# Kernel optimization log

Hardware: AMD Instinct MI355X
Metric: run time of the kernel (lower is better)

## Reference

```python
import jax, jax.numpy as jnp
import numpy as np

H = 1024      # hidden_size
NH = 16       # num heads
HD = H // NH  # head dim


def setup_inputs() -> dict:
    key = jax.random.key(0)
    ks = jax.random.split(key, 10)
    B, S = 2, 2048
    bound = 1.0 / np.sqrt(H)
    def w(k):
        return jax.random.uniform(k, (H, H), jnp.float32, -bound, bound)
    def b(k):
        return jax.random.uniform(k, (H,), jnp.float32, -bound, bound)
    return {
        "hidden_states": jax.random.normal(ks[0], (B, S, H), jnp.float32),
        "attention_mask": jnp.zeros((B, 1, 1, S), jnp.float32),
        "wq": w(ks[1]), "bq": b(ks[2]),
        "wk": w(ks[3]), "bk": b(ks[4]),
        "wv": w(ks[5]), "bv": b(ks[6]),
        "wo": w(ks[7]), "bo": b(ks[8]),
    }


def reference(hidden_states, attention_mask, wq, bq, wk, bk, wv, bv, wo, bo):
    B, S, _ = hidden_states.shape
    # linear layers: y = x @ W^T + b (torch F.linear convention)
    q = hidden_states @ wq.T + bq
    k = hidden_states @ wk.T + bk
    v = hidden_states @ wv.T + bv
    # [B, NH, S, HD]
    q = q.reshape(B, S, NH, HD).transpose(0, 2, 1, 3)
    k = k.reshape(B, S, NH, HD).transpose(0, 2, 1, 3)
    v = v.reshape(B, S, NH, HD).transpose(0, 2, 1, 3)
    scores = jnp.einsum("bhqd,bhkd->bhqk", q, k) / jnp.sqrt(jnp.float32(HD))
    scores = scores + attention_mask
    probs = jax.nn.softmax(scores, axis=-1)  # dropout_p=0 -> no dropout
    ctx = jnp.einsum("bhqk,bhkd->bhqd", probs, v)
    ctx = ctx.transpose(0, 2, 1, 3).reshape(B, S, H)
    return ctx @ wo.T + bo
```

## Files before the change

### kernel.cpp

```cpp
#include <hip/hip_runtime.h>
#include <hip/hip_bf16.h>

typedef unsigned short u16;
typedef __attribute__((ext_vector_type(4))) float f32x4;
typedef __attribute__((ext_vector_type(8))) __bf16 bf16x8;

#define NH 16
#define HD 64
#define HID 1024
#define SS 2048
#define MM 4096

__device__ __forceinline__ u16 f2b(float f) {
  unsigned u = __builtin_bit_cast(unsigned, f);
  u += 0x7fff + ((u >> 16) & 1);
  return (u16)(u >> 16);
}

__device__ __forceinline__ float fexp2(float x) {
#if __has_builtin(__builtin_amdgcn_exp2f)
  return __builtin_amdgcn_exp2f(x);
#else
  return exp2f(x);
#endif
}

template <int CTRL>
__device__ __forceinline__ float dpp_mv(float x) {
  int xi = __builtin_bit_cast(int, x);
  int yi = __builtin_amdgcn_update_dpp(xi, xi, CTRL, 0xF, 0xF, true);
  return __builtin_bit_cast(float, yi);
}
__device__ __forceinline__ float dppmax16(float v) {
  v = fmaxf(v, dpp_mv<0xB1>(v));
  v = fmaxf(v, dpp_mv<0x4E>(v));
  v = fmaxf(v, dpp_mv<0x141>(v));
  v = fmaxf(v, dpp_mv<0x140>(v));
  return v;
}
__device__ __forceinline__ float dppsum16(float v) {
  v += dpp_mv<0xB1>(v);
  v += dpp_mv<0x4E>(v);
  v += dpp_mv<0x141>(v);
  v += dpp_mv<0x140>(v);
  return v;
}

__device__ __forceinline__ void gl_lds16(const u16* g, u16* l) {
  __builtin_amdgcn_global_load_lds(
      (const __attribute__((address_space(1))) void*)g,
      (__attribute__((address_space(3))) void*)l, 16, 0, 0);
}

__global__ void cvt4(const float* __restrict__ src, u16* __restrict__ dst, int n4) {
  int i = blockIdx.x * 256 + threadIdx.x;
  if (i >= n4) return;
  float4 v = reinterpret_cast<const float4*>(src)[i];
  ushort4 o;
  o.x = f2b(v.x); o.y = f2b(v.y); o.z = f2b(v.z); o.w = f2b(v.w);
  reinterpret_cast<ushort4*>(dst)[i] = o;
}

__global__ void cvt4w(const float* __restrict__ s0, const float* __restrict__ s1,
                      const float* __restrict__ s2, const float* __restrict__ s3,
                      u16* __restrict__ d0, u16* __restrict__ d1,
                      u16* __restrict__ d2, u16* __restrict__ d3) {
  const int w = blockIdx.y;
  const float* src = (w == 0) ? s0 : (w == 1) ? s1 : (w == 2) ? s2 : s3;
  u16* dst = (w == 0) ? d0 : (w == 1) ? d1 : (w == 2) ? d2 : d3;
  int i = blockIdx.x * 256 + threadIdx.x;
  float4 v = reinterpret_cast<const float4*>(src)[i];
  ushort4 o;
  o.x = f2b(v.x); o.y = f2b(v.y); o.z = f2b(v.z); o.w = f2b(v.w);
  reinterpret_cast<ushort4*>(dst)[i] = o;
}

__global__ __launch_bounds__(256)
void gemm_qkv(const u16* __restrict__ xb,
              const u16* __restrict__ wqb, const u16* __restrict__ wkb, const u16* __restrict__ wvb,
              const float* __restrict__ bq, const float* __restrict__ bk, const float* __restrict__ bv,
              u16* __restrict__ qh, u16* __restrict__ kh, u16* __restrict__ vt) {
  const int mt = blockIdx.x;
  const int nt = blockIdx.y;
  const int wi = nt >> 3;
  const int n0 = (nt & 7) << 7;
  const int m0 = mt << 7;
  const u16* wb = (wi == 0) ? wqb : (wi == 1) ? wkb : wvb;
  const float* bias = (wi == 0) ? bq : (wi == 1) ? bk : bv;

  __shared__ u16 at[128 * 64];
  __shared__ u16 bt[128 * 64];

  const int tid = threadIdx.x;
  const int wave = tid >> 6;
  const int lane = tid & 63;
  const int g = lane >> 4;
  const int wm = (wave >> 1) << 6;
  const int wn = (wave & 1) << 6;
  const int lr = lane & 15;
  const int rb = g << 2;
  const int lrow = lane >> 3;
  const int dslot = lane & 7;

  f32x4 acc[4][4] = {};

  for (int k0 = 0; k0 < HID; k0 += 64) {
    __syncthreads();
    #pragma unroll
    for (int i = 0; i < 4; i++) {
      const int row = wave * 32 + i * 8 + lrow;
      const int scol = (dslot ^ (row & 7)) << 3;
      gl_lds16(&xb[(size_t)(m0 + row) * HID + k0 + scol], at + wave * 2048 + i * 512);
      gl_lds16(&wb[(size_t)(n0 + row) * HID + k0 + scol], bt + wave * 2048 + i * 512);
    }
    __syncthreads();
    #pragma unroll
    for (int kk = 0; kk < 2; kk++) {
      bf16x8 af[4], bfr[4];
      #pragma unroll
      for (int i = 0; i < 4; i++) {
        const int ra = wm + i * 16 + lr;
        const int rbw = wn + i * 16 + lr;
        const int sa_ = ((kk << 2) + g) ^ (ra & 7);
        const int sb_ = ((kk << 2) + g) ^ (rbw & 7);
        af[i]  = *reinterpret_cast<const bf16x8*>(&at[ra * 64 + (sa_ << 3)]);
        bfr[i] = *reinterpret_cast<const bf16x8*>(&bt[rbw * 64 + (sb_ << 3)]);
      }
      #pragma unroll
      for (int i = 0; i < 4; i++)
        #pragma unroll
        for (int j = 0; j < 4; j++)
          acc[i][j] = __builtin_amdgcn_mfma_f32_16x16x32_bf16(af[i], bfr[j], acc[i][j], 0, 0, 0);
    }
  }

  #pragma unroll
  for (int i = 0; i < 4; i++) {
    #pragma unroll
    for (int j = 0; j < 4; j++) {
      #pragma unroll
      for (int r = 0; r < 4; r++) {
        const int m = m0 + wm + i * 16 + rb + r;
        const int n = n0 + wn + j * 16 + lr;
        const float val = acc[i][j][r] + bias[n];
        const u16 bv16 = f2b(val);
        const int b = m >> 11, s = m & 2047;
        const int h = n >> 6, d = n & 63;
        if (wi == 0)      qh[((size_t)(b * NH + h) * SS + s) * HD + d] = bv16;
        else if (wi == 1) kh[((size_t)(b * NH + h) * SS + s) * HD + d] = bv16;
        else              vt[((size_t)(b * NH + h) * HD + d) * SS + s] = bv16;
      }
    }
  }
}

__global__ __launch_bounds__(256, 2)
void attn(const u16* __restrict__ qh, const u16* __restrict__ kh, const u16* __restrict__ vt,
          const float* __restrict__ mask, u16* __restrict__ ctxb) {
  const int id = blockIdx.x;
  const int bh = (id & 7) + 8 * ((id >> 3) & 3);
  const int qt = id >> 5;
  const int b = bh >> 4;
  const int h = bh & 15;
  const int q0 = qt << 7;

  const int tid = threadIdx.x;
  const int wave = tid >> 6;
  const int lane = tid & 63;
  const int g = lane >> 4;
  const int lr = lane & 15;
  const int lk = g << 3;
  const int rb = g << 2;
  const int lrow = lane >> 3;
  const int dslot = lane & 7;

  const u16* qb = qh + (size_t)bh * SS * HD;
  const u16* kb = kh + (size_t)bh * SS * HD;
  const u16* vb = vt + (size_t)bh * HD * SS;
  const float* mrow = mask + (size_t)b * SS;

  __shared__ u16 kt[2][64 * 64];
  __shared__ u16 vtile[2][64 * 64];
  __shared__ u16 pt[4][32][72];

  const int qrow0 = q0 + wave * 32;

  bf16x8 qf[2][2];
  #pragma unroll
  for (int c = 0; c < 2; c++)
    #pragma unroll
    for (int dk = 0; dk < 2; dk++)
      qf[c][dk] = *reinterpret_cast<const bf16x8*>(
          &qb[(size_t)(qrow0 + c * 16 + lr) * HD + dk * 32 + lk]);

  f32x4 o[2][4] = {};
  float mrun[2][4], lrun[2][4];
  #pragma unroll
  for (int c = 0; c < 2; c++)
    #pragma unroll
    for (int r = 0; r < 4; r++) { mrun[c][r] = -1e30f; lrun[c][r] = 0.f; }

  const float LOG2E = 1.4426950408889634f;
  const float SCL = 0.125f * LOG2E;

  auto stage = [&](u16* kdst, u16* vdst, int kv0) {
    #pragma unroll
    for (int i = 0; i < 2; i++) {
      const int row = wave * 16 + i * 8 + lrow;
      const int scol = (dslot ^ (row & 7)) << 3;
      gl_lds16(&kb[(size_t)(kv0 + row) * HD + scol], kdst + wave * 1024 + i * 512);
      gl_lds16(&vb[(size_t)row * SS + kv0 + scol], vdst + wave * 1024 + i * 512);
    }
  };

  stage(kt[0], vtile[0], 0);
  __syncthreads();

  for (int it = 0; it < SS / 64; ++it) {
    const int cur = it & 1;
    if (it + 1 < SS / 64)
      stage(kt[cur ^ 1], vtile[cur ^ 1], (it + 1) * 64);

    const int kv0 = it * 64;
    const u16* kc = kt[cur];
    const u16* vc = vtile[cur];

    f32x4 sa[2][4] = {};
    #pragma unroll
    for (int ks = 0; ks < 4; ks++) {
      const int row = ks * 16 + lr;
      const int s0 = g ^ (row & 7);
      const int s1 = (g + 4) ^ (row & 7);
      const bf16x8 kf0 = *reinterpret_cast<const bf16x8*>(&kc[row * 64 + (s0 << 3)]);
      const bf16x8 kf1 = *reinterpret_cast<const bf16x8*>(&kc[row * 64 + (s1 << 3)]);
      #pragma unroll
      for (int c = 0; c < 2; c++) {
        sa[c][ks] = __builtin_amdgcn_mfma_f32_16x16x32_bf16(qf[c][0], kf0, sa[c][ks], 0, 0, 0);
        sa[c][ks] = __builtin_amdgcn_mfma_f32_16x16x32_bf16(qf[c][1], kf1, sa[c][ks], 0, 0, 0);
      }
    }

    float mk2[4];
    #pragma unroll
    for (int ks = 0; ks < 4; ks++) mk2[ks] = mrow[kv0 + ks * 16 + lr] * LOG2E;

    float tmax[2][4];
    #pragma unroll
    for (int c = 0; c < 2; c++) {
      #pragma unroll
      for (int r = 0; r < 4; r++) tmax[c][r] = -1e30f;
      #pragma unroll
      for (int ks = 0; ks < 4; ks++)
        #pragma unroll
        for (int r = 0; r < 4; r++) {
          const float v = fmaf(sa[c][ks][r], SCL, mk2[ks]);
          sa[c][ks][r] = v;
          tmax[c][r] = fmaxf(tmax[c][r], v);
        }
      #pragma unroll
      for (int r = 0; r < 4; r++) tmax[c][r] = dppmax16(tmax[c][r]);
    }

    float need = -1e30f;
    #pragma unroll
    for (int c = 0; c < 2; c++)
      #pragma unroll
      for (int r = 0; r < 4; r++) need = fmaxf(need, tmax[c][r] - mrun[c][r]);
    if (!__all(need <= 4.0f)) {
      #pragma unroll
      for (int c = 0; c < 2; c++)
        #pragma unroll
        for (int r = 0; r < 4; r++) {
          const float mnew = fmaxf(mrun[c][r], tmax[c][r]);
          const float alpha = fexp2(mrun[c][r] - mnew);
          mrun[c][r] = mnew;
          lrun[c][r] *= alpha;
          #pragma unroll
          for (int ds = 0; ds < 4; ds++) o[c][ds][r] *= alpha;
        }
    }

    #pragma unroll
    for (int c = 0; c < 2; c++) {
      float ts[4] = {0.f, 0.f, 0.f, 0.f};
      #pragma unroll
      for (int ks = 0; ks < 4; ks++)
        #pragma unroll
        for (int r = 0; r < 4; r++) {
          const float p = fexp2(sa[c][ks][r] - mrun[c][r]);
          sa[c][ks][r] = p;
          ts[r] += p;
        }
      #pragma unroll
      for (int r = 0; r < 4; r++)
        lrun[c][r] += dppsum16(ts[r]);
      #pragma unroll
      for (int ks = 0; ks < 4; ks++)
        #pragma unroll
        for (int r = 0; r < 4; r++)
          pt[wave][c * 16 + rb + r][ks * 16 + lr] = f2b(sa[c][ks][r]);
    }

    bf16x8 pa[2][2];
    #pragma unroll
    for (int c = 0; c < 2; c++)
      #pragma unroll
      for (int ko = 0; ko < 2; ko++)
        pa[c][ko] = *reinterpret_cast<const bf16x8*>(&pt[wave][c * 16 + lr][ko * 32 + lk]);

    #pragma unroll
    for (int ds = 0; ds < 4; ds++) {
      #pragma unroll
      for (int ko = 0; ko < 2; ko++) {
        const int vrow = ds * 16 + lr;
        const int vs = ((ko << 2) + g) ^ (vrow & 7);
        const bf16x8 vf = *reinterpret_cast<const bf16x8*>(&vc[vrow * 64 + (vs << 3)]);
        #pragma unroll
        for (int c = 0; c < 2; c++)
          o[c][ds] = __builtin_amdgcn_mfma_f32_16x16x32_bf16(pa[c][ko], vf, o[c][ds], 0, 0, 0);
      }
    }
    __syncthreads();
  }

  #pragma unroll
  for (int c = 0; c < 2; c++) {
    float inv[4];
    #pragma unroll
    for (int r = 0; r < 4; r++) inv[r] = 1.0f / lrun[c][r];
    #pragma unroll
    for (int ds = 0; ds < 4; ds++)
      #pragma unroll
      for (int r = 0; r < 4; r++) {
        const int srow = qrow0 + c * 16 + rb + r;
        ctxb[(size_t)(b * SS + srow) * HID + h * HD + ds * 16 + lr] = f2b(o[c][ds][r] * inv[r]);
      }
  }
}

__global__ __launch_bounds__(256)
void gemm_out(const u16* __restrict__ ab, const u16* __restrict__ wb,
              const float* __restrict__ bias, float* __restrict__ out) {
  const int m0 = blockIdx.x << 7;
  const int n0 = blockIdx.y << 6;

  __shared__ u16 at[128 * 32];
  __shared__ u16 bt[64 * 32];

  const int tid = threadIdx.x;
  const int wave = tid >> 6;
  const int lane = tid & 63;
  const int wm = wave << 5;
  const int lr = lane & 15;
  const int lk = (lane >> 4) << 3;
  const int rb = (lane >> 4) << 2;

  const int srow = wave * 32 + (lane >> 2);
  const int brow = wave * 16 + (lane >> 2);
  const int scol = (lane & 3) << 3;
  const size_t ga0 = (size_t)(m0 + srow) * HID + scol;
  const size_t gb0 = (size_t)(n0 + brow) * HID + scol;
  u16* la0 = at + wave * 1024;
  u16* lb0 = bt + wave * 512;

  f32x4 acc[2][4] = {};

  for (int k0 = 0; k0 < HID; k0 += 32) {
    __syncthreads();
    gl_lds16(&ab[ga0 + k0], la0);
    gl_lds16(&ab[ga0 + 16 * HID + k0], la0 + 512);
    gl_lds16(&wb[gb0 + k0], lb0);
    __syncthreads();
    bf16x8 af[2], bfr[4];
    #pragma unroll
    for (int i = 0; i < 2; i++)
      af[i] = *reinterpret_cast<const bf16x8*>(&at[(wm + i * 16 + lr) * 32 + lk]);
    #pragma unroll
    for (int j = 0; j < 4; j++)
      bfr[j] = *reinterpret_cast<const bf16x8*>(&bt[(j * 16 + lr) * 32 + lk]);
    #pragma unroll
    for (int i = 0; i < 2; i++)
      #pragma unroll
      for (int j = 0; j < 4; j++)
        acc[i][j] = __builtin_amdgcn_mfma_f32_16x16x32_bf16(af[i], bfr[j], acc[i][j], 0, 0, 0);
  }

  #pragma unroll
  for (int i = 0; i < 2; i++)
    #pragma unroll
    for (int j = 0; j < 4; j++)
      #pragma unroll
      for (int r = 0; r < 4; r++) {
        const int m = m0 + wm + i * 16 + rb + r;
        const int n = n0 + j * 16 + lr;
        out[(size_t)m * HID + n] = acc[i][j][r] + bias[n];
      }
}

extern "C" void kernel_launch(void* const* d_in, const int* in_sizes, int n_in,
                              void* d_out, int out_size, void* d_ws, size_t ws_size,
                              hipStream_t stream) {
  const float* hs   = (const float*)d_in[0];
  const float* mask = (const float*)d_in[1];
  const float* wq   = (const float*)d_in[2];
  const float* bq   = (const float*)d_in[3];
  const float* wk   = (const float*)d_in[4];
  const float* bk   = (const float*)d_in[5];
  const float* wv   = (const float*)d_in[6];
  const float* bv   = (const float*)d_in[7];
  const float* wo   = (const float*)d_in[8];
  const float* bo   = (const float*)d_in[9];
  float* out = (float*)d_out;

  char* ws = (char*)d_ws;
  u16* xb   = (u16*)(ws);
  u16* ctxb = (u16*)(ws + ((size_t)8  << 20));
  u16* qhb  = (u16*)(ws + ((size_t)16 << 20));
  u16* khb  = (u16*)(ws + ((size_t)24 << 20));
  u16* vtb  = (u16*)(ws + ((size_t)32 << 20));
  u16* wqb  = (u16*)(ws + ((size_t)40 << 20));
  u16* wkb  = (u16*)(ws + ((size_t)42 << 20));
  u16* wvb  = (u16*)(ws + ((size_t)44 << 20));
  u16* wob  = (u16*)(ws + ((size_t)46 << 20));

  cvt4<<<4096, 256, 0, stream>>>(hs, xb, MM * HID / 4);
  cvt4w<<<dim3(1024, 4), 256, 0, stream>>>(wq, wk, wv, wo, wqb, wkb, wvb, wob);

  gemm_qkv<<<dim3(32, 24), 256, 0, stream>>>(xb, wqb, wkb, wvb, bq, bk, bv, qhb, khb, vtb);
  attn<<<512, 256, 0, stream>>>(qhb, khb, vtb, mask, ctxb);
  gemm_out<<<dim3(32, 16), 256, 0, stream>>>(ctxb, wob, bo, out);
}
```

Baseline: 162.3 us.

## Defer softmax row reductions and widen output GEMM K-tile with swizzled LDS

In the attention kernel, the cross-lane row max is computed only when the rescale branch fires. The row sum is kept per lane and reduced once at the end, and P is written to shared memory directly without the temporary. The output projection GEMM now loads 64-wide K tiles into XOR-swizzled LDS, halving loop iterations and barriers and avoiding bank conflicts. The intent is to cut DPP reduction work and synchronization overhead, at the price of more LDS use. The rescale check now runs on lane-local maxima, which looks safe because the full row max is recomputed when the branch is taken.

```diff
diff --git a/kernel.cpp b/kernel.cpp
--- a/kernel.cpp
+++ b/kernel.cpp
@@ -257,8 +257,6 @@
           sa[c][ks][r] = v;
           tmax[c][r] = fmaxf(tmax[c][r], v);
         }
-      #pragma unroll
-      for (int r = 0; r < 4; r++) tmax[c][r] = dppmax16(tmax[c][r]);
     }
 
     float need = -1e30f;
@@ -271,7 +269,8 @@
       for (int c = 0; c < 2; c++)
         #pragma unroll
         for (int r = 0; r < 4; r++) {
-          const float mnew = fmaxf(mrun[c][r], tmax[c][r]);
+          const float rowmax = dppmax16(tmax[c][r]);
+          const float mnew = fmaxf(mrun[c][r], rowmax);
           const float alpha = fexp2(mrun[c][r] - mnew);
           mrun[c][r] = mnew;
           lrun[c][r] *= alpha;
@@ -281,25 +280,15 @@
     }
 
     #pragma unroll
-    for (int c = 0; c < 2; c++) {
-      float ts[4] = {0.f, 0.f, 0.f, 0.f};
+    for (int c = 0; c < 2; c++)
       #pragma unroll
       for (int ks = 0; ks < 4; ks++)
         #pragma unroll
         for (int r = 0; r < 4; r++) {
           const float p = fexp2(sa[c][ks][r] - mrun[c][r]);
-          sa[c][ks][r] = p;
-          ts[r] += p;
+          lrun[c][r] += p;
+          pt[wave][c * 16 + rb + r][ks * 16 + lr] = f2b(p);
         }
-      #pragma unroll
-      for (int r = 0; r < 4; r++)
-        lrun[c][r] += dppsum16(ts[r]);
-      #pragma unroll
-      for (int ks = 0; ks < 4; ks++)
-        #pragma unroll
-        for (int r = 0; r < 4; r++)
-          pt[wave][c * 16 + rb + r][ks * 16 + lr] = f2b(sa[c][ks][r]);
-    }
 
     bf16x8 pa[2][2];
     #pragma unroll
@@ -327,7 +316,7 @@
   for (int c = 0; c < 2; c++) {
     float inv[4];
     #pragma unroll
-    for (int r = 0; r < 4; r++) inv[r] = 1.0f / lrun[c][r];
+    for (int r = 0; r < 4; r++) inv[r] = 1.0f / dppsum16(lrun[c][r]);
     #pragma unroll
     for (int ds = 0; ds < 4; ds++)
       #pragma unroll
@@ -344,45 +333,57 @@
   const int m0 = blockIdx.x << 7;
   const int n0 = blockIdx.y << 6;
 
-  __shared__ u16 at[128 * 32];
-  __shared__ u16 bt[64 * 32];
+  __shared__ u16 at[128 * 64];
+  __shared__ u16 bt[64 * 64];
 
   const int tid = threadIdx.x;
   const int wave = tid >> 6;
   const int lane = tid & 63;
+  const int g = lane >> 4;
   const int wm = wave << 5;
   const int lr = lane & 15;
-  const int lk = (lane >> 4) << 3;
-  const int rb = (lane >> 4) << 2;
-
-  const int srow = wave * 32 + (lane >> 2);
-  const int brow = wave * 16 + (lane >> 2);
-  const int scol = (lane & 3) << 3;
-  const size_t ga0 = (size_t)(m0 + srow) * HID + scol;
-  const size_t gb0 = (size_t)(n0 + brow) * HID + scol;
-  u16* la0 = at + wave * 1024;
-  u16* lb0 = bt + wave * 512;
+  const int rb = g << 2;
+  const int lrow = lane >> 3;
+  const int dslot = lane & 7;
 
   f32x4 acc[2][4] = {};
 
-  for (int k0 = 0; k0 < HID; k0 += 32) {
+  for (int k0 = 0; k0 < HID; k0 += 64) {
     __syncthreads();
-    gl_lds16(&ab[ga0 + k0], la0);
-    gl_lds16(&ab[ga0 + 16 * HID + k0], la0 + 512);
-    gl_lds16(&wb[gb0 + k0], lb0);
+    #pragma unroll
+    for (int i = 0; i < 4; i++) {
+      const int row = wave * 32 + i * 8 + lrow;
+      const int scol = (dslot ^ (row & 7)) << 3;
+      gl_lds16(&ab[(size_t)(m0 + row) * HID + k0 + scol], at + wave * 2048 + i * 512);
+    }
+    #pragma unroll
+    for (int i = 0; i < 2; i++) {
+      const int row = wave * 16 + i * 8 + lrow;
+      const int scol = (dslot ^ (row & 7)) << 3;
+      gl_lds16(&wb[(size_t)(n0 + row) * HID + k0 + scol], bt + wave * 1024 + i * 512);
+    }
     __syncthreads();
-    bf16x8 af[2], bfr[4];
-    #pragma unroll
-    for (int i = 0; i < 2; i++)
-      af[i] = *reinterpret_cast<const bf16x8*>(&at[(wm + i * 16 + lr) * 32 + lk]);
-    #pragma unroll
-    for (int j = 0; j < 4; j++)
-      bfr[j] = *reinterpret_cast<const bf16x8*>(&bt[(j * 16 + lr) * 32 + lk]);
-    #pragma unroll
-    for (int i = 0; i < 2; i++)
-      #pragma unroll
-      for (int j = 0; j < 4; j++)
-        acc[i][j] = __builtin_amdgcn_mfma_f32_16x16x32_bf16(af[i], bfr[j], acc[i][j], 0, 0, 0);
+    #pragma unroll
+    for (int kk = 0; kk < 2; kk++) {
+      bf16x8 af[2], bfr[4];
+      #pragma unroll
+      for (int i = 0; i < 2; i++) {
+        const int ra = wm + i * 16 + lr;
+        const int sa_ = ((kk << 2) + g) ^ (ra & 7);
+        af[i] = *reinterpret_cast<const bf16x8*>(&at[ra * 64 + (sa_ << 3)]);
+      }
+      #pragma unroll
+      for (int j = 0; j < 4; j++) {
+        const int rbw = j * 16 + lr;
+        const int sb_ = ((kk << 2) + g) ^ (rbw & 7);
+        bfr[j] = *reinterpret_cast<const bf16x8*>(&bt[rbw * 64 + (sb_ << 3)]);
+      }
+      #pragma unroll
+      for (int i = 0; i < 2; i++)
+        #pragma unroll
+        for (int j = 0; j < 4; j++)
+          acc[i][j] = __builtin_amdgcn_mfma_f32_16x16x32_bf16(af[i], bfr[j], acc[i][j], 0, 0, 0);
+    }
   }
 
   #pragma unroll
```

Result: faster. 144.7 us (-10.8%).
